# Kernel tuning notes

Measured on AMD Instinct MI355X. Metric: run time of the kernel, lower is better.

Reference implementation:

```python
import jax, jax.numpy as jnp
import numpy as np

NUM_TOKENS = 2048
HIDDEN = 2048
INTERM = 768
NUM_EXPERTS = 16
TOP_K = 8


def setup_inputs() -> dict:
    key = jax.random.key(0)
    k1, k2, k3, k4, k5 = jax.random.split(key, 5)
    hidden_states = jax.random.normal(k1, (NUM_TOKENS, HIDDEN), dtype=jnp.float32)
    # scale weights ~N(0, 0.02) like typical transformer init to keep activations sane
    gate_up_proj = jax.random.normal(k2, (NUM_EXPERTS, HIDDEN, 2 * INTERM), dtype=jnp.float32) * 0.02
    down_proj = jax.random.normal(k3, (NUM_EXPERTS, INTERM, HIDDEN), dtype=jnp.float32) * 0.02
    expert_indices = jax.random.randint(k4, (NUM_TOKENS, TOP_K), 0, NUM_EXPERTS, dtype=jnp.int32)
    expert_weights = jax.random.uniform(k5, (NUM_TOKENS, TOP_K), dtype=jnp.float32)
    return {
        "hidden_states": hidden_states,
        "gate_up_proj": gate_up_proj,
        "down_proj": down_proj,
        "expert_indices": expert_indices,
        "expert_weights": expert_weights,
    }


def reference(hidden_states, gate_up_proj, down_proj, expert_indices, expert_weights):
    T, H = hidden_states.shape
    E, _, I2 = gate_up_proj.shape
    I = I2 // 2
    # Dense dispatch over the (small, fixed) expert axis -- same math as the
    # per-token top-k fallback, vectorized. gate_up: [T, E, 2I]
    gate_up = jnp.einsum("th,ehi->tei", hidden_states, gate_up_proj)
    gate, up = gate_up[..., :I], gate_up[..., I:]
    activated = jax.nn.silu(gate) * up                      # [T, E, I]
    expert_out = jnp.einsum("tei,eih->teh", activated, down_proj)  # [T, E, H]
    # Per-token routing weights scattered onto the dense expert axis: [T, E]
    combine = jnp.zeros((T, E), dtype=hidden_states.dtype)
    combine = combine.at[jnp.arange(T)[:, None], expert_indices].add(expert_weights)
    output = jnp.einsum("te,teh->th", combine, expert_out)  # [T, H]
    return output
```

## Files before the change

kernel.cpp:

```cpp
#include <hip/hip_runtime.h>
#include <hip/hip_bf16.h>

#define T_TOK 2048
#define HID 2048
#define IMED 768
#define NEXP 16
#define TOPK 8
#define MAXPAIR (T_TOK * TOPK)

using f32x4  = __attribute__((ext_vector_type(4))) float;
using bf16x8 = __attribute__((ext_vector_type(8))) __bf16;

__device__ __forceinline__ f32x4 mfma16(bf16x8 a, bf16x8 b, f32x4 c) {
  return __builtin_amdgcn_mfma_f32_16x16x32_bf16(a, b, c, 0, 0, 0);
}

__device__ __forceinline__ void gload16(const void* g, void* lds) {
  __builtin_amdgcn_global_load_lds((const __attribute__((address_space(1))) unsigned int*)g,
                                   (__attribute__((address_space(3))) unsigned int*)lds,
                                   16, 0, 0);
}

__global__ void moe_cvt_x(const float* __restrict__ X, __bf16* __restrict__ XB) {
  int i = (blockIdx.x * blockDim.x + threadIdx.x) * 8;
  float4 v0 = *(const float4*)&X[i];
  float4 v1 = *(const float4*)&X[i + 4];
  bf16x8 o;
  o[0] = (__bf16)v0.x; o[1] = (__bf16)v0.y; o[2] = (__bf16)v0.z; o[3] = (__bf16)v0.w;
  o[4] = (__bf16)v1.x; o[5] = (__bf16)v1.y; o[6] = (__bf16)v1.z; o[7] = (__bf16)v1.w;
  *(bf16x8*)&XB[i] = o;
}

__global__ __launch_bounds__(256) void moe_transpose(const float* __restrict__ in,
                                                     __bf16* __restrict__ out,
                                                     int R, int C) {
  __shared__ __bf16 tile[64][66];
  const int e = blockIdx.z;
  const float* ib = in + (size_t)e * R * C;
  __bf16* ob = out + (size_t)e * R * C;
  const int c0 = blockIdx.x * 64, r0 = blockIdx.y * 64;
  const int tid = threadIdx.x;
  const int lr = tid >> 4;
  const int lc = (tid & 15) * 4;
#pragma unroll
  for (int i = 0; i < 4; ++i) {
    int r = lr + i * 16;
    float4 v = *(const float4*)&ib[(size_t)(r0 + r) * C + c0 + lc];
    tile[r][lc + 0] = (__bf16)v.x; tile[r][lc + 1] = (__bf16)v.y;
    tile[r][lc + 2] = (__bf16)v.z; tile[r][lc + 3] = (__bf16)v.w;
  }
  __syncthreads();
  const int oc = tid >> 2;
  const int sr = (tid & 3) * 16;
  bf16x8 o0, o1;
#pragma unroll
  for (int j = 0; j < 8; ++j) o0[j] = tile[sr + j][oc];
#pragma unroll
  for (int j = 0; j < 8; ++j) o1[j] = tile[sr + 8 + j][oc];
  *(bf16x8*)&ob[(size_t)(c0 + oc) * R + r0 + sr] = o0;
  *(bf16x8*)&ob[(size_t)(c0 + oc) * R + r0 + sr + 8] = o1;
}

__global__ void moe_route_build(const int* __restrict__ idx, const float* __restrict__ wgt,
                                float* __restrict__ combine, int* __restrict__ meta) {
  int t = blockIdx.x * blockDim.x + threadIdx.x;
  if (t >= T_TOK) return;
  float c[NEXP];
#pragma unroll
  for (int e = 0; e < NEXP; ++e) c[e] = 0.f;
  for (int k = 0; k < TOPK; ++k) c[idx[t * TOPK + k]] += wgt[t * TOPK + k];
  for (int e = 0; e < NEXP; ++e) {
    combine[t * NEXP + e] = c[e];
    if (c[e] != 0.f) atomicAdd(&meta[e], 1);
  }
}

__global__ void moe_scan(int* __restrict__ meta) {
  if (threadIdx.x == 0 && blockIdx.x == 0) {
    int s = 0;
    for (int e = 0; e < NEXP; ++e) { meta[16 + e] = s; meta[33 + e] = s; s += meta[e]; }
    meta[32] = s;
  }
}

__global__ void moe_scatter(const float* __restrict__ combine, int* __restrict__ meta,
                            int* __restrict__ route_tok, float* __restrict__ route_w) {
  int t = blockIdx.x * blockDim.x + threadIdx.x;
  if (t >= T_TOK) return;
  for (int e = 0; e < NEXP; ++e) {
    float c = combine[t * NEXP + e];
    if (c != 0.f) {
      int p = atomicAdd(&meta[33 + e], 1);
      route_tok[p] = t;
      route_w[p] = c;
    }
  }
}

__global__ __launch_bounds__(256) void moe_gemm1(
    const __bf16* __restrict__ XB, const __bf16* __restrict__ WguT,
    const int* __restrict__ rtok, const float* __restrict__ rw,
    const int* __restrict__ meta, __bf16* __restrict__ ACT) {
  const int orig = blockIdx.x;
  const int wgid = (orig & 7) * 384 + (orig >> 3);
  const int mx = wgid & 15;
  const int ny = (wgid >> 4) % 12;
  const int e  = wgid / 192;

  const int seg0 = meta[16 + e];
  const int cnt  = meta[16 + e + 1] - seg0;
  const int m0 = mx * 128;
  if (m0 >= cnt) return;
  const int n0 = ny * 64;

  __shared__ char As[2][16384];
  __shared__ char Bs[2][16384];

  const int tid = threadIdx.x;
  const int l = tid & 63;
  const int w = tid >> 6;
  const int wm = w >> 1, wn = w & 1;
  const int swoff = 16 * ((l & 7) ^ (l >> 3));

  const char* baseA[4];
  const char* baseB[4];
#pragma unroll
  for (int q = 0; q < 4; ++q) {
    const int r = (w * 4 + q) * 8 + (l >> 3);
    int grow = m0 + r; if (grow >= cnt) grow = cnt - 1;
    const int tok = rtok[seg0 + grow];
    baseA[q] = (const char*)(XB + (size_t)tok * HID) + swoff;
    const int sec = r >> 6, s = r & 63;
    const int wrow = (s < 32) ? (n0 + sec * 32 + s) : (IMED + n0 + sec * 32 + (s - 32));
    baseB[q] = (const char*)(WguT + ((size_t)e * (2 * IMED) + wrow) * HID) + swoff;
  }

  f32x4 acc[4][4];
  const f32x4 zero = {0.f, 0.f, 0.f, 0.f};
#pragma unroll
  for (int i = 0; i < 4; ++i)
#pragma unroll
    for (int j = 0; j < 4; ++j) acc[i][j] = zero;

  auto STAGE = [&](int buf, int k0b) {
#pragma unroll
    for (int q = 0; q < 4; ++q) {
      gload16(baseA[q] + k0b, &As[buf][(w * 4 + q) * 1024]);
      gload16(baseB[q] + k0b, &Bs[buf][(w * 4 + q) * 1024]);
    }
  };
  auto COMPUTE = [&](int buf) {
#pragma unroll
    for (int ks = 0; ks < 2; ++ks) {
      const int colb = ks * 64 + (l >> 4) * 16;
      bf16x8 af[4], bf[4];
#pragma unroll
      for (int mi = 0; mi < 4; ++mi) {
        const int row = wm * 64 + mi * 16 + (l & 15);
        af[mi] = *(const bf16x8*)&As[buf][row * 128 + (colb ^ ((row & 7) << 4))];
      }
#pragma unroll
      for (int ni = 0; ni < 4; ++ni) {
        const int row = wn * 64 + ni * 16 + (l & 15);
        bf[ni] = *(const bf16x8*)&Bs[buf][row * 128 + (colb ^ ((row & 7) << 4))];
      }
#pragma unroll
      for (int mi = 0; mi < 4; ++mi)
#pragma unroll
        for (int ni = 0; ni < 4; ++ni)
          acc[mi][ni] = mfma16(af[mi], bf[ni], acc[mi][ni]);
    }
  };

  STAGE(0, 0);
  __syncthreads();
  int cur = 0;
  for (int t = 1; t < HID / 64; ++t) {
    STAGE(cur ^ 1, t * 128);
    COMPUTE(cur);
    __syncthreads();
    cur ^= 1;
  }
  COMPUTE(cur);

  const int cbase = n0 + wn * 32;
#pragma unroll
  for (int mi = 0; mi < 4; ++mi) {
    const int rb = wm * 64 + mi * 16 + ((l >> 4) << 2);
#pragma unroll
    for (int r = 0; r < 4; ++r) {
      const int row = m0 + rb + r;
      if (row < cnt) {
        const float wgt = rw[seg0 + row];
#pragma unroll
        for (int ni = 0; ni < 2; ++ni) {
          const float g = acc[mi][ni][r];
          const float u = acc[mi][ni + 2][r];
          const float s = g / (1.f + __expf(-g));
          ACT[(size_t)(seg0 + row) * IMED + cbase + ni * 16 + (l & 15)] = (__bf16)(s * u * wgt);
        }
      }
    }
  }
}

__global__ __launch_bounds__(256) void moe_gemm2(
    const __bf16* __restrict__ ACT, const __bf16* __restrict__ WdT,
    const int* __restrict__ rtok, const int* __restrict__ meta,
    float* __restrict__ out) {
  const int orig = blockIdx.x;
  const int wgid = (orig & 7) * 512 + (orig >> 3);
  const int mx = wgid & 15;
  const int ny = (wgid >> 4) & 15;
  const int e  = wgid >> 8;

  const int seg0 = meta[16 + e];
  const int cnt  = meta[16 + e + 1] - seg0;
  const int m0 = mx * 128;
  if (m0 >= cnt) return;
  const int n0 = ny * 128;

  __shared__ char As[2][16384];
  __shared__ char Bs[2][16384];

  const int tid = threadIdx.x;
  const int l = tid & 63;
  const int w = tid >> 6;
  const int wm = w >> 1, wn = w & 1;
  const int swoff = 16 * ((l & 7) ^ (l >> 3));

  const char* baseA[4];
  const char* baseB[4];
#pragma unroll
  for (int q = 0; q < 4; ++q) {
    const int r = (w * 4 + q) * 8 + (l >> 3);
    int grow = m0 + r; if (grow >= cnt) grow = cnt - 1;
    baseA[q] = (const char*)(ACT + (size_t)(seg0 + grow) * IMED) + swoff;
    baseB[q] = (const char*)(WdT + ((size_t)e * HID + n0 + r) * IMED) + swoff;
  }

  f32x4 acc[4][4];
  const f32x4 zero = {0.f, 0.f, 0.f, 0.f};
#pragma unroll
  for (int i = 0; i < 4; ++i)
#pragma unroll
    for (int j = 0; j < 4; ++j) acc[i][j] = zero;

  auto STAGE = [&](int buf, int k0b) {
#pragma unroll
    for (int q = 0; q < 4; ++q) {
      gload16(baseA[q] + k0b, &As[buf][(w * 4 + q) * 1024]);
      gload16(baseB[q] + k0b, &Bs[buf][(w * 4 + q) * 1024]);
    }
  };
  auto COMPUTE = [&](int buf) {
#pragma unroll
    for (int ks = 0; ks < 2; ++ks) {
      const int colb = ks * 64 + (l >> 4) * 16;
      bf16x8 af[4], bf[4];
#pragma unroll
      for (int mi = 0; mi < 4; ++mi) {
        const int row = wm * 64 + mi * 16 + (l & 15);
        af[mi] = *(const bf16x8*)&As[buf][row * 128 + (colb ^ ((row & 7) << 4))];
      }
#pragma unroll
      for (int ni = 0; ni < 4; ++ni) {
        const int row = wn * 64 + ni * 16 + (l & 15);
        bf[ni] = *(const bf16x8*)&Bs[buf][row * 128 + (colb ^ ((row & 7) << 4))];
      }
#pragma unroll
      for (int mi = 0; mi < 4; ++mi)
#pragma unroll
        for (int ni = 0; ni < 4; ++ni)
          acc[mi][ni] = mfma16(af[mi], bf[ni], acc[mi][ni]);
    }
  };

  STAGE(0, 0);
  __syncthreads();
  int cur = 0;
  for (int t = 1; t < IMED / 64; ++t) {
    STAGE(cur ^ 1, t * 128);
    COMPUTE(cur);
    __syncthreads();
    cur ^= 1;
  }
  COMPUTE(cur);

#pragma unroll
  for (int mi = 0; mi < 4; ++mi) {
    const int rb = wm * 64 + mi * 16 + ((l >> 4) << 2);
#pragma unroll
    for (int r = 0; r < 4; ++r) {
      const int row = m0 + rb + r;
      if (row < cnt) {
        const int tok = rtok[seg0 + row];
#pragma unroll
        for (int ni = 0; ni < 4; ++ni)
          atomicAdd(&out[(size_t)tok * HID + n0 + wn * 64 + ni * 16 + (l & 15)],
                    acc[mi][ni][r]);
      }
    }
  }
}

extern "C" void kernel_launch(void* const* d_in, const int* in_sizes, int n_in,
                              void* d_out, int out_size, void* d_ws, size_t ws_size,
                              hipStream_t stream) {
  const float* X   = (const float*)d_in[0];
  const float* GUP = (const float*)d_in[1];
  const float* DP  = (const float*)d_in[2];
  const int*   IDX = (const int*)d_in[3];
  const float* W   = (const float*)d_in[4];
  float* out = (float*)d_out;

  size_t off = 0;
  auto alloc = [&](size_t bytes) -> void* {
    void* p = (char*)d_ws + off;
    off = (off + bytes + 255) & ~(size_t)255;
    return p;
  };
  __bf16* XB      = (__bf16*)alloc((size_t)T_TOK * HID * 2);
  __bf16* WguT    = (__bf16*)alloc((size_t)NEXP * 2 * IMED * HID * 2);
  __bf16* WdT     = (__bf16*)alloc((size_t)NEXP * HID * IMED * 2);
  __bf16* ACT     = (__bf16*)alloc((size_t)(MAXPAIR + 128) * IMED * 2);
  float*  combine = (float*)alloc((size_t)T_TOK * NEXP * 4);
  int*    meta    = (int*)alloc(64 * 4);
  int*    rtok    = (int*)alloc((size_t)MAXPAIR * 4);
  float*  rw      = (float*)alloc((size_t)MAXPAIR * 4);
  if (off > ws_size) return;

  hipMemsetAsync(meta, 0, 256, stream);
  moe_cvt_x<<<T_TOK * HID / (256 * 8), 256, 0, stream>>>(X, XB);
  moe_transpose<<<dim3((2 * IMED) / 64, HID / 64, NEXP), 256, 0, stream>>>(GUP, WguT, HID, 2 * IMED);
  moe_transpose<<<dim3(HID / 64, IMED / 64, NEXP), 256, 0, stream>>>(DP, WdT, IMED, HID);
  moe_route_build<<<T_TOK / 256, 256, 0, stream>>>(IDX, W, combine, meta);
  moe_scan<<<1, 64, 0, stream>>>(meta);
  moe_scatter<<<T_TOK / 256, 256, 0, stream>>>(combine, meta, rtok, rw);
  hipMemsetAsync(d_out, 0, (size_t)T_TOK * HID * 4, stream);
  moe_gemm1<<<3072, 256, 0, stream>>>(XB, WguT, rtok, rw, meta, ACT);
  moe_gemm2<<<4096, 256, 0, stream>>>(ACT, WdT, rtok, meta, out);
}
```

Measured before the change: 396.3 us.

## Replace output atomics with per-pair bf16 buffer and deterministic combine kernel

The down-projection GEMM now writes each routed pair's result as bf16 into a scratch buffer (reusing the gate/up weight buffer) instead of atomically adding into the fp32 output. A new per-token combine kernel sums a token's pairs via a slot index recorded during scatter, which removes the output memset and the atomic contention. The transpose kernel also stages fp32 in shared memory with vector stores. The cost is extra traffic for the intermediate buffer and bf16 rounding of per-expert outputs before summation.

```diff
diff --git a/kernel.cpp b/kernel.cpp
--- a/kernel.cpp
+++ b/kernel.cpp
@@ -34,7 +34,7 @@
 __global__ __launch_bounds__(256) void moe_transpose(const float* __restrict__ in,
                                                      __bf16* __restrict__ out,
                                                      int R, int C) {
-  __shared__ __bf16 tile[64][66];
+  __shared__ __align__(16) float tile[64][68];
   const int e = blockIdx.z;
   const float* ib = in + (size_t)e * R * C;
   __bf16* ob = out + (size_t)e * R * C;
@@ -46,17 +46,16 @@
   for (int i = 0; i < 4; ++i) {
     int r = lr + i * 16;
     float4 v = *(const float4*)&ib[(size_t)(r0 + r) * C + c0 + lc];
-    tile[r][lc + 0] = (__bf16)v.x; tile[r][lc + 1] = (__bf16)v.y;
-    tile[r][lc + 2] = (__bf16)v.z; tile[r][lc + 3] = (__bf16)v.w;
+    *(float4*)&tile[r][lc] = v;
   }
   __syncthreads();
   const int oc = tid >> 2;
   const int sr = (tid & 3) * 16;
   bf16x8 o0, o1;
 #pragma unroll
-  for (int j = 0; j < 8; ++j) o0[j] = tile[sr + j][oc];
-#pragma unroll
-  for (int j = 0; j < 8; ++j) o1[j] = tile[sr + 8 + j][oc];
+  for (int j = 0; j < 8; ++j) o0[j] = (__bf16)tile[sr + j][oc];
+#pragma unroll
+  for (int j = 0; j < 8; ++j) o1[j] = (__bf16)tile[sr + 8 + j][oc];
   *(bf16x8*)&ob[(size_t)(c0 + oc) * R + r0 + sr] = o0;
   *(bf16x8*)&ob[(size_t)(c0 + oc) * R + r0 + sr + 8] = o1;
 }
@@ -84,17 +83,22 @@
 }
 
 __global__ void moe_scatter(const float* __restrict__ combine, int* __restrict__ meta,
-                            int* __restrict__ route_tok, float* __restrict__ route_w) {
+                            int* __restrict__ route_tok, float* __restrict__ route_w,
+                            int* __restrict__ ptok, int* __restrict__ pcnt) {
   int t = blockIdx.x * blockDim.x + threadIdx.x;
   if (t >= T_TOK) return;
+  int slot = 0;
   for (int e = 0; e < NEXP; ++e) {
     float c = combine[t * NEXP + e];
     if (c != 0.f) {
       int p = atomicAdd(&meta[33 + e], 1);
       route_tok[p] = t;
       route_w[p] = c;
-    }
-  }
+      ptok[t * TOPK + slot] = p;
+      ++slot;
+    }
+  }
+  pcnt[t] = slot;
 }
 
 __global__ __launch_bounds__(256) void moe_gemm1(
@@ -206,8 +210,7 @@
 
 __global__ __launch_bounds__(256) void moe_gemm2(
     const __bf16* __restrict__ ACT, const __bf16* __restrict__ WdT,
-    const int* __restrict__ rtok, const int* __restrict__ meta,
-    float* __restrict__ out) {
+    const int* __restrict__ meta, __bf16* __restrict__ ACT2) {
   const int orig = blockIdx.x;
   const int wgid = (orig & 7) * 512 + (orig >> 3);
   const int mx = wgid & 15;
@@ -294,14 +297,35 @@
     for (int r = 0; r < 4; ++r) {
       const int row = m0 + rb + r;
       if (row < cnt) {
-        const int tok = rtok[seg0 + row];
 #pragma unroll
         for (int ni = 0; ni < 4; ++ni)
-          atomicAdd(&out[(size_t)tok * HID + n0 + wn * 64 + ni * 16 + (l & 15)],
-                    acc[mi][ni][r]);
-      }
-    }
-  }
+          ACT2[(size_t)(seg0 + row) * HID + n0 + wn * 64 + ni * 16 + (l & 15)] =
+              (__bf16)acc[mi][ni][r];
+      }
+    }
+  }
+}
+
+__global__ __launch_bounds__(256) void moe_combine(const __bf16* __restrict__ ACT2,
+                                                   const int* __restrict__ ptok,
+                                                   const int* __restrict__ pcnt,
+                                                   float* __restrict__ out) {
+  const int t = blockIdx.x;
+  const int h = threadIdx.x * 8;
+  const int n = pcnt[t];
+  float a[8];
+#pragma unroll
+  for (int j = 0; j < 8; ++j) a[j] = 0.f;
+  for (int k = 0; k < n; ++k) {
+    const int p = ptok[t * TOPK + k];
+    bf16x8 v = *(const bf16x8*)&ACT2[(size_t)p * HID + h];
+#pragma unroll
+    for (int j = 0; j < 8; ++j) a[j] += (float)v[j];
+  }
+  float4 o0 = {a[0], a[1], a[2], a[3]};
+  float4 o1 = {a[4], a[5], a[6], a[7]};
+  *(float4*)&out[(size_t)t * HID + h] = o0;
+  *(float4*)&out[(size_t)t * HID + h + 4] = o1;
 }
 
 extern "C" void kernel_launch(void* const* d_in, const int* in_sizes, int n_in,
@@ -328,7 +352,11 @@
   int*    meta    = (int*)alloc(64 * 4);
   int*    rtok    = (int*)alloc((size_t)MAXPAIR * 4);
   float*  rw      = (float*)alloc((size_t)MAXPAIR * 4);
+  int*    ptok    = (int*)alloc((size_t)T_TOK * TOPK * 4);
+  int*    pcnt    = (int*)alloc((size_t)T_TOK * 4);
   if (off > ws_size) return;
+
+  __bf16* ACT2 = WguT;
 
   hipMemsetAsync(meta, 0, 256, stream);
   moe_cvt_x<<<T_TOK * HID / (256 * 8), 256, 0, stream>>>(X, XB);
@@ -336,8 +364,8 @@
   moe_transpose<<<dim3(HID / 64, IMED / 64, NEXP), 256, 0, stream>>>(DP, WdT, IMED, HID);
   moe_route_build<<<T_TOK / 256, 256, 0, stream>>>(IDX, W, combine, meta);
   moe_scan<<<1, 64, 0, stream>>>(meta);
-  moe_scatter<<<T_TOK / 256, 256, 0, stream>>>(combine, meta, rtok, rw);
-  hipMemsetAsync(d_out, 0, (size_t)T_TOK * HID * 4, stream);
+  moe_scatter<<<T_TOK / 256, 256, 0, stream>>>(combine, meta, rtok, rw, ptok, pcnt);
   moe_gemm1<<<3072, 256, 0, stream>>>(XB, WguT, rtok, rw, meta, ACT);
-  moe_gemm2<<<4096, 256, 0, stream>>>(ACT, WdT, rtok, meta, out);
-}
+  moe_gemm2<<<4096, 256, 0, stream>>>(ACT, WdT, meta, ACT2);
+  moe_combine<<<T_TOK, 256, 0, stream>>>(ACT2, ptok, pcnt, out);
+}
```

Result: faster. 340.7 us (-14.0%).
